# Performance work log

Measured on AMD Instinct MI355X. Metric: run time of the kernel, lower is better.

The kernel has to match this reference:

```python
import jax, jax.numpy as jnp
import numpy as np
jax.config.update("jax_enable_x64", True)

T_OLD = 60000
T_NEW = 60000
NV = 30000
MAX_STEPS = 300
FB_CHUNK = 500  # T_OLD must be divisible by this

FACE_OPP = np.array([[1, 2, 3], [0, 2, 3], [0, 1, 3], [0, 1, 2]])
EDGES = [(0, 1), (0, 2), (0, 3), (1, 2), (1, 3), (2, 3)]


def setup_inputs() -> dict:
    key = jax.random.key(0)
    k1, k2, k3, k4, k5 = jax.random.split(key, 5)
    # distinct vertices per tet (sorted base + strictly increasing offsets)
    off = jnp.arange(4, dtype=jnp.int64)
    new_indices = jnp.sort(jax.random.randint(k1, (T_NEW, 4), 0, NV - 4, dtype=jnp.int64), axis=1) + off
    old_indices = jnp.sort(jax.random.randint(k2, (T_OLD, 4), 0, NV - 4, dtype=jnp.int64), axis=1) + off
    return {
        "new_indices": new_indices,
        "old_indices": old_indices,
        "old_cc": jax.random.normal(k3, (T_OLD, 3), dtype=jnp.float32),
        "new_cc": jax.random.normal(k4, (T_NEW, 3), dtype=jnp.float32),
        "vertex_positions": jax.random.uniform(k5, (NV, 3), dtype=jnp.float32),
    }


def _min_edge_length(verts, indices):
    p = verts[indices]  # (T,4,3)
    el = jnp.stack([jnp.linalg.norm(p[:, a] - p[:, b], axis=-1) for a, b in EDGES])
    return el.min(axis=0)


def _forward(new_indices, old_indices, old_cc, new_cc, vertex_positions):
    T_new = new_indices.shape[0]
    T_old = old_indices.shape[0]
    Vn = vertex_positions.shape[0]

    # --- 1. unchanged-tet detection via sorted-vertex int64 keys ---
    key4 = lambda s: ((s[:, 0] * Vn + s[:, 1]) * Vn + s[:, 2]) * Vn + s[:, 3]
    ok = key4(jnp.sort(old_indices, axis=1))
    nk = key4(jnp.sort(new_indices, axis=1))
    order = jnp.argsort(ok)
    sk = ok[order]
    pos = jnp.searchsorted(sk, nk, side='right') - 1
    posc = jnp.clip(pos, 0, T_old - 1)
    matched = jnp.where((pos >= 0) & (sk[posc] == nk), order[posc], -1)
    is_matched = matched >= 0
    matched_safe = jnp.maximum(matched, 0)

    # --- 2. face adjacency of old mesh (sorted face keys, adjacent-equal pairing) ---
    fi = jnp.sort(old_indices[:, FACE_OPP], axis=2)          # (T_old,4,3)
    fk = (fi[..., 0] * Vn + fi[..., 1]) * Vn + fi[..., 2]    # (T_old,4)
    all_keys = fk.T.reshape(-1)                              # f-major like the numpy concat
    all_tets = jnp.tile(jnp.arange(T_old), 4)
    all_locals = jnp.repeat(jnp.arange(4), T_old)
    o2 = jnp.argsort(all_keys)
    sk2, st, sl = all_keys[o2], all_tets[o2], all_locals[o2]
    same = sk2[:-1] == sk2[1:]
    neighbors = jnp.full((T_old, 4), -1, dtype=jnp.int64)
    neighbors = neighbors.at[jnp.where(same, st[:-1], T_old), sl[:-1]].set(st[1:], mode='drop')
    neighbors = neighbors.at[jnp.where(same, st[1:], T_old), sl[1:]].set(st[:-1], mode='drop')

    # --- 3. per-old-tet inverse edge matrix; degenerate tets get no neighbors ---
    verts = jax.lax.stop_gradient(vertex_positions).astype(jnp.float32)
    p = verts[old_indices]                                   # (T_old,4,3)
    v0 = p[:, 0]
    Tm = jnp.stack([p[:, 1] - v0, p[:, 2] - v0, p[:, 3] - v0], axis=-1)
    degen = jnp.abs(jnp.linalg.det(Tm)) < 1e-10
    Tinv = jnp.linalg.inv(jnp.where(degen[:, None, None], jnp.eye(3, dtype=Tm.dtype), Tm))
    neighbors = jnp.where(degen[:, None], -1, neighbors)

    prio = jnp.full((Vn,), -1, dtype=jnp.int64)
    ar = jnp.arange(T_old)
    for vi in range(4):
        prio = prio.at[old_indices[:, vi]].max(vi * T_old + ar)
    v2t = jnp.where(prio >= 0, prio % T_old, 0)

    # --- 5. barycentric walk (masked, all float inputs stop-gradiented; int outputs) ---
    cent = jax.lax.stop_gradient(verts[new_indices].mean(axis=1))  # (T_new,3)
    seed = v2t[new_indices[:, 0]]
    n_walk = jnp.sum(~is_matched)
    thr = jnp.maximum(jnp.int64(100), n_walk // 1000)

    def cond(state):
        step, cur, rem, act = state
        return (step < MAX_STEPS) & (jnp.sum(act) >= thr)

    def body(state):
        step, cur, rem, act = state
        rel = cent - v0[cur]
        bary = jnp.einsum('nij,nj->ni', Tinv[cur], rel)
        all_b = jnp.concatenate([(1.0 - bary.sum(axis=1))[:, None], bary], axis=1)
        conv = act & (all_b.min(axis=1) >= -1e-4)
        rem = jnp.where(conv, cur, rem)
        act = act & ~conv
        nb = neighbors[cur, jnp.argmin(all_b, axis=1)]
        at_bd = act & (nb < 0)
        rem = jnp.where(at_bd, cur, rem)
        act = act & ~at_bd
        cur = jnp.where(act, nb, cur)
        return (step + 1, cur, rem, act)

    _, cur, rem, act = jax.lax.while_loop(cond, body, (jnp.int64(0), seed, seed, ~is_matched))
    rem = jnp.where(act, cur, rem)

    # --- 6. nearest-centroid fallback for unfinished walks (gated, chunked) ---
    old_cents = jax.lax.stop_gradient(verts[old_indices].mean(axis=1))

    def fallback(_):
        p2 = (cent ** 2).sum(-1)
        c2 = (old_cents ** 2).sum(-1)
        def scan_body(carry, i):
            bd, bi = carry
            c = jax.lax.dynamic_slice(old_cents, (i * FB_CHUNK, 0), (FB_CHUNK, 3))
            cn = jax.lax.dynamic_slice(c2, (i * FB_CHUNK,), (FB_CHUNK,))
            d = p2[:, None] - 2.0 * (cent @ c.T) + cn[None, :]
            md = d.min(axis=1)
            mi = d.argmin(axis=1).astype(jnp.int64) + i * FB_CHUNK
            imp = md < bd
            return (jnp.where(imp, md, bd), jnp.where(imp, mi, bi)), None
        init = (jnp.full((T_new,), jnp.inf, dtype=jnp.float32), jnp.zeros((T_new,), dtype=jnp.int64))
        (bd, bi), _ = jax.lax.scan(scan_body, init, jnp.arange(T_old // FB_CHUNK))
        return bi

    fb = jax.lax.cond(jnp.sum(act) > 0, fallback, lambda _: jnp.zeros((T_new,), dtype=jnp.int64), None)
    rem = jnp.clip(jnp.where(act, fb, rem), 0, T_old - 1)
    remap = jnp.where(is_matched, matched_safe, rem)

    # --- 7. candidates: containing tet + 4 face neighbors ---
    face_nb = neighbors[remap]
    face_nb = jnp.where(face_nb >= 0, face_nb, remap[:, None])
    cands = jnp.concatenate([remap[:, None], face_nb], axis=1)            # (T_new,5)
    cands = jnp.where(is_matched[:, None], matched_safe[:, None], cands)

    # --- 8. overlap / circumcenter-distance weights ---
    cand_verts = old_indices[cands]                                       # (T_new,5,4)
    overlap = (cand_verts[:, :, :, None] == new_indices[:, None, None, :]).any(-1).sum(-1).astype(jnp.float32)
    cc_d2 = ((old_cc[cands] - new_cc[:, None, :]) ** 2).sum(-1)
    raw = jnp.exp(overlap * 2.0) / (cc_d2 + 1e-8)
    weights = raw / raw.sum(axis=1, keepdims=True)

    # --- 9. density scale: min-edge-length ratio ---
    old_el = _min_edge_length(vertex_positions, old_indices)[cands]
    new_el = _min_edge_length(vertex_positions, new_indices)
    density_scale = jnp.clip(old_el / jnp.maximum(new_el[:, None], 1e-8), 0.1, 10.0)

    return cands, weights, density_scale


_forward_jit = jax.jit(_forward)


def reference(new_indices, old_indices, old_cc, new_cc, vertex_positions):
    return _forward_jit(new_indices, old_indices, old_cc, new_cc, vertex_positions)
```

## Files before the change

### kernel.cpp

```cpp
#include <hip/hip_runtime.h>

#pragma clang fp contract(off)

#define TOLD 60000
#define TNEW 60000
#define NVERT 30000
#define MAXSTEPS 300
#define THSZ 131072
#define FHSZ 131072
#define EMPTY64 0xFFFFFFFFFFFFFFFFULL

#define NB_SETUP 235
#define NB_NEWG  235
#define NB_FACE  938
#define NB_MATCH 235
#define NB_FB    120
#define FBRANGE  (TNEW / NB_FB)

#define OFF_TKEYS    0u
#define OFF_FTAB     1048576u
#define OFF_NBR      2097152u
#define OFF_PRIO     3057152u
#define FF_BYTES     3177152u
#define OFF_CNT      3177152u
#define OFF_TVALS    3179200u
#define OFF_IDXOLD   3703552u
#define OFF_SSTEP    4663552u
#define OFF_DEGEN    4903552u
#define OFF_MATCHED  5143552u
#define OFF_TV4      5383552u
#define OFF_COLD4    8263552u
#define OFF_CNEW4    9223552u
#define OFF_DM       10183552u

struct P {
  const unsigned int* rawNew;
  const unsigned int* rawOld;
  const float* occ;
  const float* ncc;
  const float* verts;
  float* out;
  unsigned long long* tkeys;
  unsigned long long* ftab;
  int* counters;
  int* tvals;
  int* idxOld;
  int* nbr;
  int* prio;
  int* sstep;
  int* degen;
  int* matched;
  float4* Tv4;
  float4* cold4;
  float4* cnew4;
  unsigned long long* dm;
  unsigned int dmMask;
};

__device__ __forceinline__ unsigned hash64(unsigned long long k){
  k ^= k >> 33; k *= 0xff51afd7ed558ccdULL;
  k ^= k >> 33; k *= 0xc4ceb9fe1a85ec53ULL;
  k ^= k >> 33;
  return (unsigned)k;
}
__device__ __forceinline__ void cswap(int& a, int& b){ if (a > b){ int t = a; a = b; b = t; } }

__device__ __forceinline__ int detect64(const unsigned int* raw){
  unsigned acc = 0;
  const uint4* r4 = (const uint4*)raw;
  #pragma unroll
  for (int k = 0; k < 32; ++k){ uint4 v = r4[k]; acc |= (v.y | v.w); }
  return acc == 0u;
}

__device__ __forceinline__ int4 load_tet4(const unsigned int* raw, int is64, int t){
  if (is64){
    uint4 a = ((const uint4*)raw)[t * 2 + 0];
    uint4 b = ((const uint4*)raw)[t * 2 + 1];
    return make_int4((int)a.x, (int)a.z, (int)b.x, (int)b.z);
  }
  uint4 a = ((const uint4*)raw)[t];
  return make_int4((int)a.x, (int)a.y, (int)a.z, (int)a.w);
}

__device__ __forceinline__ void face_insert(unsigned long long* ftab, int* nbr,
                                            unsigned long long fkey, int t, int l){
  unsigned long long mine = (fkey << 18) | (unsigned long long)(t * 4 + l);
  unsigned slot = hash64(fkey ^ 0x9e3779b97f4a7c15ULL) & (FHSZ - 1);
  while (true){
    unsigned long long prev = atomicCAS(&ftab[slot], EMPTY64, mine);
    if (prev == EMPTY64) return;
    if ((prev >> 18) == fkey){
      int oid = (int)(prev & 0x3FFFFULL);
      nbr[t * 4 + l] = oid >> 2;
      nbr[oid] = t;
      return;
    }
    slot = (slot + 1) & (FHSZ - 1);
  }
}

__device__ __forceinline__ float min_edge_r(
    float q0x, float q0y, float q0z, float q1x, float q1y, float q1z,
    float q2x, float q2y, float q2z, float q3x, float q3y, float q3z){
  float m = 3.402823466e+38f;
  float dx, dy, dz, d;
  dx = q0x - q1x; dy = q0y - q1y; dz = q0z - q1z; d = sqrtf((dx*dx + dy*dy) + dz*dz); m = fminf(m, d);
  dx = q0x - q2x; dy = q0y - q2y; dz = q0z - q2z; d = sqrtf((dx*dx + dy*dy) + dz*dz); m = fminf(m, d);
  dx = q0x - q3x; dy = q0y - q3y; dz = q0z - q3z; d = sqrtf((dx*dx + dy*dy) + dz*dz); m = fminf(m, d);
  dx = q1x - q2x; dy = q1y - q2y; dz = q1z - q2z; d = sqrtf((dx*dx + dy*dy) + dz*dz); m = fminf(m, d);
  dx = q1x - q3x; dy = q1y - q3y; dz = q1z - q3z; d = sqrtf((dx*dx + dy*dy) + dz*dz); m = fminf(m, d);
  dx = q2x - q3x; dy = q2y - q3y; dz = q2z - q3z; d = sqrtf((dx*dx + dy*dy) + dz*dz); m = fminf(m, d);
  return m;
}

__global__ __launch_bounds__(256) void k_front(P p){
  int bb = blockIdx.x;
  if (bb < NB_SETUP){
    int t = bb * 256 + threadIdx.x;
    if (bb == 0){
      for (int j = threadIdx.x; j < 384; j += 256) p.counters[j] = 0;
    }
    if (t >= TOLD) return;
    int is64 = detect64(p.rawOld);
    int4 iv4 = load_tet4(p.rawOld, is64, t);
    int i0 = iv4.x, i1 = iv4.y, i2 = iv4.z, i3 = iv4.w;
    ((int4*)p.idxOld)[t] = iv4;

    atomicMax(&p.prio[i0], 0 * TOLD + t);
    atomicMax(&p.prio[i1], 1 * TOLD + t);
    atomicMax(&p.prio[i2], 2 * TOLD + t);
    atomicMax(&p.prio[i3], 3 * TOLD + t);

    {
      int s0 = i0, s1 = i1, s2 = i2, s3 = i3;
      cswap(s0, s1); cswap(s2, s3); cswap(s0, s2); cswap(s1, s3); cswap(s1, s2);
      unsigned long long key =
          (unsigned long long)((((long long)s0 * NVERT + s1) * NVERT + s2) * NVERT + s3);
      unsigned slot = hash64(key) & (THSZ - 1);
      while (true){
        unsigned long long prev = atomicCAS(&p.tkeys[slot], EMPTY64, key);
        if (prev == EMPTY64){ p.tvals[slot] = t; break; }
        if (prev == key){ atomicMax(&p.tvals[slot], t); break; }
        slot = (slot + 1) & (THSZ - 1);
      }
    }

    if (p.dmMask){
      const int FO[4][3] = {{1, 2, 3}, {0, 2, 3}, {0, 1, 3}, {0, 1, 2}};
      int iv[4] = {i0, i1, i2, i3};
      #pragma unroll
      for (int l = 0; l < 4; ++l){
        int a = iv[FO[l][0]], b = iv[FO[l][1]], c = iv[FO[l][2]];
        cswap(a, b); cswap(a, c); cswap(b, c);
        unsigned long long fk = (unsigned long long)(((long long)a * NVERT + b) * NVERT + c);
        p.dm[hash64(fk) & p.dmMask] = (fk << 18) | (unsigned long long)(t * 4 + l);
      }
    }

    float q0x = p.verts[i0 * 3 + 0], q0y = p.verts[i0 * 3 + 1], q0z = p.verts[i0 * 3 + 2];
    float q1x = p.verts[i1 * 3 + 0], q1y = p.verts[i1 * 3 + 1], q1z = p.verts[i1 * 3 + 2];
    float q2x = p.verts[i2 * 3 + 0], q2y = p.verts[i2 * 3 + 1], q2z = p.verts[i2 * 3 + 2];
    float q3x = p.verts[i3 * 3 + 0], q3y = p.verts[i3 * 3 + 1], q3z = p.verts[i3 * 3 + 2];
    float e1x = q1x - q0x, e1y = q1y - q0y, e1z = q1z - q0z;
    float e2x = q2x - q0x, e2y = q2y - q0y, e2z = q2z - q0z;
    float e3x = q3x - q0x, e3y = q3y - q0y, e3z = q3z - q0z;
    float c23x = e2y * e3z - e2z * e3y;
    float c23y = e2z * e3x - e2x * e3z;
    float c23z = e2x * e3y - e2y * e3x;
    float det = e1x * c23x + e1y * c23y + e1z * c23z;
    int dg = (fabsf(det) < 1e-10f) ? 1 : 0;
    p.degen[t] = dg;
    float4 r0, r1, r2;
    if (dg){
      r0 = make_float4(1.f, 0.f, 0.f, q0x);
      r1 = make_float4(0.f, 1.f, 0.f, q0y);
      r2 = make_float4(0.f, 0.f, 1.f, q0z);
    } else {
      float inv = 1.0f / det;
      float c31x = e3y * e1z - e3z * e1y;
      float c31y = e3z * e1x - e3x * e1z;
      float c31z = e3x * e1y - e3y * e1x;
      float c12x = e1y * e2z - e1z * e2y;
      float c12y = e1z * e2x - e1x * e2z;
      float c12z = e1x * e2y - e1y * e2x;
      r0 = make_float4(c23x * inv, c23y * inv, c23z * inv, q0x);
      r1 = make_float4(c31x * inv, c31y * inv, c31z * inv, q0y);
      r2 = make_float4(c12x * inv, c12y * inv, c12z * inv, q0z);
    }
    p.Tv4[t * 3 + 0] = r0;
    p.Tv4[t * 3 + 1] = r1;
    p.Tv4[t * 3 + 2] = r2;
    float el = min_edge_r(q0x, q0y, q0z, q1x, q1y, q1z, q2x, q2y, q2z, q3x, q3y, q3z);
    p.cold4[t] = make_float4((((q0x + q1x) + q2x) + q3x) * 0.25f,
                             (((q0y + q1y) + q2y) + q3y) * 0.25f,
                             (((q0z + q1z) + q2z) + q3z) * 0.25f, el);
  } else {
    int n = (bb - NB_SETUP) * 256 + threadIdx.x;
    if (n >= TNEW) return;
    int is64 = detect64(p.rawNew);
    int4 ni = load_tet4(p.rawNew, is64, n);
    float q0x = p.verts[ni.x * 3 + 0], q0y = p.verts[ni.x * 3 + 1], q0z = p.verts[ni.x * 3 + 2];
    float q1x = p.verts[ni.y * 3 + 0], q1y = p.verts[ni.y * 3 + 1], q1z = p.verts[ni.y * 3 + 2];
    float q2x = p.verts[ni.z * 3 + 0], q2y = p.verts[ni.z * 3 + 1], q2z = p.verts[ni.z * 3 + 2];
    float q3x = p.verts[ni.w * 3 + 0], q3y = p.verts[ni.w * 3 + 1], q3z = p.verts[ni.w * 3 + 2];
    float el = min_edge_r(q0x, q0y, q0z, q1x, q1y, q1z, q2x, q2y, q2z, q3x, q3y, q3z);
    p.cnew4[n] = make_float4((((q0x + q1x) + q2x) + q3x) * 0.25f,
                             (((q0y + q1y) + q2y) + q3y) * 0.25f,
                             (((q0z + q1z) + q2z) + q3z) * 0.25f, el);
  }
}

__global__ __launch_bounds__(256) void k_mid(P p){
  int bb = blockIdx.x;
  if (bb < NB_FACE){
    int i = bb * 256 + threadIdx.x;
    if (i >= TOLD * 4) return;
    int t = i >> 2, l = i & 3;
    int4 iv4 = ((const int4*)p.idxOld)[t];
    int iv[4] = {iv4.x, iv4.y, iv4.z, iv4.w};
    const int FO[4][3] = {{1, 2, 3}, {0, 2, 3}, {0, 1, 3}, {0, 1, 2}};
    int a = iv[FO[l][0]], b = iv[FO[l][1]], c = iv[FO[l][2]];
    cswap(a, b); cswap(a, c); cswap(b, c);
    unsigned long long fk = (unsigned long long)(((long long)a * NVERT + b) * NVERT + c);
    if (p.dmMask){
      unsigned long long mine = (fk << 18) | (unsigned long long)i;
      unsigned long long got = p.dm[hash64(fk) & p.dmMask];
      if (got == mine) return;
      if ((got >> 18) == fk){
        int wid = (int)(got & 0x3FFFFULL);
        p.nbr[i] = wid >> 2;
        p.nbr[wid] = t;
        return;
      }
    }
    face_insert(p.ftab, p.nbr, fk, t, l);
  } else {
    int n = (bb - NB_FACE) * 256 + threadIdx.x;
    if (n >= TNEW) return;
    int is64 = detect64(p.rawNew);
    int4 ni = load_tet4(p.rawNew, is64, n);
    int s0 = ni.x, s1 = ni.y, s2 = ni.z, s3 = ni.w;
    cswap(s0, s1); cswap(s2, s3); cswap(s0, s2); cswap(s1, s3); cswap(s1, s2);
    unsigned long long key =
        (unsigned long long)((((long long)s0 * NVERT + s1) * NVERT + s2) * NVERT + s3);
    int m = -1;
    unsigned slot = hash64(key) & (THSZ - 1);
    while (true){
      unsigned long long k = p.tkeys[slot];
      if (k == EMPTY64) break;
      if (k == key){ m = p.tvals[slot]; break; }
      slot = (slot + 1) & (THSZ - 1);
    }
    p.matched[n] = m;
  }
}

__device__ __forceinline__ void assemble_walker(const P& p, int n, int m, int remap){
  int cds[5];
  if (m >= 0){
    cds[0] = cds[1] = cds[2] = cds[3] = cds[4] = m;
  } else {
    cds[0] = remap;
    int dg = p.degen[remap];
    int4 nb4 = ((const int4*)p.nbr)[remap];
    int nbl[4] = {nb4.x, nb4.y, nb4.z, nb4.w};
    for (int l = 0; l < 4; ++l){
      int fb = dg ? -1 : nbl[l];
      cds[1 + l] = (fb >= 0) ? fb : remap;
    }
  }
  bool same = (cds[1] == cds[0]) & (cds[2] == cds[0]) &
              (cds[3] == cds[0]) & (cds[4] == cds[0]);
  int is64 = detect64(p.rawNew);
  int4 ni = load_tet4(p.rawNew, is64, n);
  float nc0 = p.ncc[n * 3 + 0], nc1 = p.ncc[n * 3 + 1], nc2 = p.ncc[n * 3 + 2];
  float nelv = fmaxf(p.cnew4[n].w, 1e-8f);
  if (same){
    int ct = cds[0];
    int4 cv = ((const int4*)p.idxOld)[ct];
    int ov = 0;
    ov += (cv.x == ni.x || cv.x == ni.y || cv.x == ni.z || cv.x == ni.w) ? 1 : 0;
    ov += (cv.y == ni.x || cv.y == ni.y || cv.y == ni.z || cv.y == ni.w) ? 1 : 0;
    ov += (cv.z == ni.x || cv.z == ni.y || cv.z == ni.z || cv.z == ni.w) ? 1 : 0;
    ov += (cv.w == ni.x || cv.w == ni.y || cv.w == ni.z || cv.w == ni.w) ? 1 : 0;
    float d0 = p.occ[ct * 3 + 0] - nc0;
    float d1 = p.occ[ct * 3 + 1] - nc1;
    float d2 = p.occ[ct * 3 + 2] - nc2;
    float ccd2 = (d0 * d0 + d1 * d1) + d2 * d2;
    float raw = expf((float)ov * 2.0f) / (ccd2 + 1e-8f);
    float rsum = 0.0f;
    rsum += raw; rsum += raw; rsum += raw; rsum += raw; rsum += raw;
    float wgt = raw / rsum;
    float ds = p.cold4[ct].w / nelv;
    ds = fminf(fmaxf(ds, 0.1f), 10.0f);
    float cf = (float)ct;
    for (int c = 0; c < 5; ++c){
      p.out[n * 5 + c] = cf;
      p.out[TNEW * 5 + n * 5 + c] = wgt;
      p.out[2 * TNEW * 5 + n * 5 + c] = ds;
    }
    return;
  }
  float raws[5]; float rsum = 0.0f;
  float oels[5];
  for (int c = 0; c < 5; ++c){
    int ct = cds[c];
    int4 cv = ((const int4*)p.idxOld)[ct];
    int ov = 0;
    ov += (cv.x == ni.x || cv.x == ni.y || cv.x == ni.z || cv.x == ni.w) ? 1 : 0;
    ov += (cv.y == ni.x || cv.y == ni.y || cv.y == ni.z || cv.y == ni.w) ? 1 : 0;
    ov += (cv.z == ni.x || cv.z == ni.y || cv.z == ni.z || cv.z == ni.w) ? 1 : 0;
    ov += (cv.w == ni.x || cv.w == ni.y || cv.w == ni.z || cv.w == ni.w) ? 1 : 0;
    float d0 = p.occ[ct * 3 + 0] - nc0;
    float d1 = p.occ[ct * 3 + 1] - nc1;
    float d2 = p.occ[ct * 3 + 2] - nc2;
    float ccd2 = (d0 * d0 + d1 * d1) + d2 * d2;
    float raw = expf((float)ov * 2.0f) / (ccd2 + 1e-8f);
    raws[c] = raw; rsum += raw;
    oels[c] = p.cold4[ct].w;
  }
  for (int c = 0; c < 5; ++c){
    p.out[n * 5 + c] = (float)cds[c];
    p.out[TNEW * 5 + n * 5 + c] = raws[c] / rsum;
    float ds = oels[c] / nelv;
    ds = fminf(fmaxf(ds, 0.1f), 10.0f);
    p.out[2 * TNEW * 5 + n * 5 + c] = ds;
  }
}

__global__ __launch_bounds__(256) void k_walkall(P p){
  __shared__ int s_hist[MAXSTEPS + 2];
  __shared__ int s_nw;
  for (int j = threadIdx.x; j < MAXSTEPS + 2; j += 256) s_hist[j] = 0;
  if (threadIdx.x == 0) s_nw = 0;
  __syncthreads();
  int n = blockIdx.x * blockDim.x + threadIdx.x;
  if (n < TNEW){
    int m = p.matched[n];
    if (m >= 0){
      assemble_walker(p, n, m, 0);
    } else {
      atomicAdd(&s_nw, 1);
      int is64 = detect64(p.rawNew);
      int i0 = is64 ? (int)((const long long*)p.rawNew)[n * 4] : ((const int*)p.rawNew)[n * 4];
      int pr = p.prio[i0];
      int c = (pr >= 0) ? (pr % TOLD) : 0;
      float4 cn = p.cnew4[n];
      int s = MAXSTEPS + 1;
      for (int k = 1; k <= MAXSTEPS; ++k){
        float4 r0 = p.Tv4[c * 3 + 0];
        float4 r1 = p.Tv4[c * 3 + 1];
        float4 r2 = p.Tv4[c * 3 + 2];
        float rx = cn.x - r0.w, ry = cn.y - r1.w, rz = cn.z - r2.w;
        float b0 = r0.x * rx + r0.y * ry + r0.z * rz;
        float b1 = r1.x * rx + r1.y * ry + r1.z * rz;
        float b2 = r2.x * rx + r2.y * ry + r2.z * rz;
        float a0 = 1.0f - (b0 + b1 + b2);
        float ab[4] = {a0, b0, b1, b2};
        int amin = 0; float mn = ab[0];
        for (int j = 1; j < 4; ++j){ if (ab[j] < mn){ mn = ab[j]; amin = j; } }
        if (mn >= -0.0001f){ s = k; break; }
        int nb = p.degen[c] ? -1 : p.nbr[c * 4 + amin];
        if (nb < 0){ s = k; break; }
        c = nb;
      }
      p.sstep[n] = s;
      atomicAdd(&s_hist[s], 1);
      assemble_walker(p, n, -1, c);
    }
  }
  __syncthreads();
  if (threadIdx.x == 0 && s_nw) atomicAdd(&p.counters[0], s_nw);
  for (int j = threadIdx.x; j < MAXSTEPS + 2; j += 256){
    int v = s_hist[j];
    if (v) atomicAdd(&p.counters[64 + j], v);
  }
}

__device__ __forceinline__ int compute_S(const int* counters){
  int nw = counters[0];
  int thr = max(100, nw / 1000);
  if (nw < thr) return 0;
  int cnt = nw;
  for (int k = 1; k <= MAXSTEPS; ++k){
    cnt -= counters[64 + k];
    if (cnt < thr) return k;
  }
  return MAXSTEPS;
}

__global__ __launch_bounds__(256) void k_tail(P p){
  __shared__ float sd[256];
  __shared__ int si[256];
  __shared__ int s_hits[256];
  __shared__ int s_nhits;
  __shared__ int s_S;
  if (threadIdx.x == 0) s_S = compute_S(p.counters);
  __syncthreads();
  int S = s_S;
  int base = blockIdx.x * FBRANGE;
  for (int chunk = base; chunk < base + FBRANGE; chunk += 256){
    if (threadIdx.x == 0) s_nhits = 0;
    __syncthreads();
    int n = chunk + threadIdx.x;
    if (n < base + FBRANGE && n < TNEW){
      if (p.matched[n] < 0 && p.sstep[n] > S)
        s_hits[atomicAdd(&s_nhits, 1)] = n;
    }
    __syncthreads();
    int nh = s_nhits;
    for (int h = 0; h < nh; ++h){
      int n2 = s_hits[h];
      float4 cn = p.cnew4[n2];
      float cx = cn.x, cy = cn.y, cz = cn.z;
      float p2 = (cx * cx + cy * cy) + cz * cz;
      float bd = 3.402823466e+38f; int bi = 0;
      for (int j = threadIdx.x; j < TOLD; j += 256){
        float4 oc = p.cold4[j];
        float dot = (cx * oc.x + cy * oc.y) + cz * oc.z;
        float c2 = (oc.x * oc.x + oc.y * oc.y) + oc.z * oc.z;
        float d = (p2 - 2.0f * dot) + c2;
        if (d < bd || (d == bd && j < bi)){ bd = d; bi = j; }
      }
      sd[threadIdx.x] = bd; si[threadIdx.x] = bi;
      __syncthreads();
      for (int s = 128; s > 0; s >>= 1){
        if ((int)threadIdx.x < s){
          float od = sd[threadIdx.x + s]; int oi = si[threadIdx.x + s];
          if (od < sd[threadIdx.x] || (od == sd[threadIdx.x] && oi < si[threadIdx.x])){
            sd[threadIdx.x] = od; si[threadIdx.x] = oi;
          }
        }
        __syncthreads();
      }
      if (threadIdx.x == 0){
        int r = si[0];
        if (r < 0) r = 0; if (r > TOLD - 1) r = TOLD - 1;
        assemble_walker(p, n2, -1, r);
      }
      __syncthreads();
    }
    __syncthreads();
  }
}

extern "C" void kernel_launch(void* const* d_in, const int* in_sizes, int n_in,
                              void* d_out, int out_size, void* d_ws, size_t ws_size,
                              hipStream_t stream) {
  char* w = (char*)d_ws;
  P p;
  p.rawNew = (const unsigned int*)d_in[0];
  p.rawOld = (const unsigned int*)d_in[1];
  p.occ    = (const float*)d_in[2];
  p.ncc    = (const float*)d_in[3];
  p.verts  = (const float*)d_in[4];
  p.out    = (float*)d_out;
  p.tkeys    = (unsigned long long*)(w + OFF_TKEYS);
  p.ftab     = (unsigned long long*)(w + OFF_FTAB);
  p.nbr      = (int*)(w + OFF_NBR);
  p.prio     = (int*)(w + OFF_PRIO);
  p.counters = (int*)(w + OFF_CNT);
  p.tvals    = (int*)(w + OFF_TVALS);
  p.idxOld   = (int*)(w + OFF_IDXOLD);
  p.sstep    = (int*)(w + OFF_SSTEP);
  p.degen    = (int*)(w + OFF_DEGEN);
  p.matched  = (int*)(w + OFF_MATCHED);
  p.Tv4      = (float4*)(w + OFF_TV4);
  p.cold4    = (float4*)(w + OFF_COLD4);
  p.cnew4    = (float4*)(w + OFF_CNEW4);
  p.dm       = (unsigned long long*)(w + OFF_DM);
  size_t avail = (ws_size > (size_t)OFF_DM) ? ws_size - (size_t)OFF_DM : 0;
  unsigned dmMask = 0;
  for (int bshift = 21; bshift >= 16; --bshift){
    if (avail >= ((size_t)8 << bshift)){ dmMask = (1u << bshift) - 1u; break; }
  }
  p.dmMask = dmMask;

  hipMemsetAsync(w, 0xFF, FF_BYTES, stream);
  hipLaunchKernelGGL(k_front,   dim3(NB_SETUP + NB_NEWG), dim3(256), 0, stream, p);
  hipLaunchKernelGGL(k_mid,     dim3(NB_FACE + NB_MATCH), dim3(256), 0, stream, p);
  hipLaunchKernelGGL(k_walkall, dim3((TNEW + 255) / 256), dim3(256), 0, stream, p);
  hipLaunchKernelGGL(k_tail,    dim3(NB_FB), dim3(256), 0, stream, p);
}
```

Measured before the change: 116.5 us.

## Fold workspace memset into front kernel and move tet matching into walk kernel

```diff
diff --git a/kernel.cpp b/kernel.cpp
--- a/kernel.cpp
+++ b/kernel.cpp
@@ -12,8 +12,9 @@
 
 #define NB_SETUP 235
 #define NB_NEWG  235
+#define NB_INIT  194
 #define NB_FACE  938
-#define NB_MATCH 235
+#define NB_WALK  235
 #define NB_FB    120
 #define FBRANGE  (TNEW / NB_FB)
 
@@ -22,12 +23,12 @@
 #define OFF_NBR      2097152u
 #define OFF_PRIO     3057152u
 #define FF_BYTES     3177152u
+#define FF_UINT4     198572u
 #define OFF_CNT      3177152u
 #define OFF_TVALS    3179200u
 #define OFF_IDXOLD   3703552u
 #define OFF_SSTEP    4663552u
 #define OFF_DEGEN    4903552u
-#define OFF_MATCHED  5143552u
 #define OFF_TV4      5383552u
 #define OFF_COLD4    8263552u
 #define OFF_CNEW4    9223552u
@@ -49,7 +50,6 @@
   int* prio;
   int* sstep;
   int* degen;
-  int* matched;
   float4* Tv4;
   float4* cold4;
   float4* cnew4;
@@ -117,34 +117,15 @@
 __global__ __launch_bounds__(256) void k_front(P p){
   int bb = blockIdx.x;
   if (bb < NB_SETUP){
-    int t = bb * 256 + threadIdx.x;
     if (bb == 0){
       for (int j = threadIdx.x; j < 384; j += 256) p.counters[j] = 0;
     }
+    int t = bb * 256 + threadIdx.x;
     if (t >= TOLD) return;
     int is64 = detect64(p.rawOld);
     int4 iv4 = load_tet4(p.rawOld, is64, t);
     int i0 = iv4.x, i1 = iv4.y, i2 = iv4.z, i3 = iv4.w;
     ((int4*)p.idxOld)[t] = iv4;
-
-    atomicMax(&p.prio[i0], 0 * TOLD + t);
-    atomicMax(&p.prio[i1], 1 * TOLD + t);
-    atomicMax(&p.prio[i2], 2 * TOLD + t);
-    atomicMax(&p.prio[i3], 3 * TOLD + t);
-
-    {
-      int s0 = i0, s1 = i1, s2 = i2, s3 = i3;
-      cswap(s0, s1); cswap(s2, s3); cswap(s0, s2); cswap(s1, s3); cswap(s1, s2);
-      unsigned long long key =
-          (unsigned long long)((((long long)s0 * NVERT + s1) * NVERT + s2) * NVERT + s3);
-      unsigned slot = hash64(key) & (THSZ - 1);
-      while (true){
-        unsigned long long prev = atomicCAS(&p.tkeys[slot], EMPTY64, key);
-        if (prev == EMPTY64){ p.tvals[slot] = t; break; }
-        if (prev == key){ atomicMax(&p.tvals[slot], t); break; }
-        slot = (slot + 1) & (THSZ - 1);
-      }
-    }
 
     if (p.dmMask){
       const int FO[4][3] = {{1, 2, 3}, {0, 2, 3}, {0, 1, 3}, {0, 1, 2}};
@@ -195,7 +176,7 @@
     p.cold4[t] = make_float4((((q0x + q1x) + q2x) + q3x) * 0.25f,
                              (((q0y + q1y) + q2y) + q3y) * 0.25f,
                              (((q0z + q1z) + q2z) + q3z) * 0.25f, el);
-  } else {
+  } else if (bb < NB_SETUP + NB_NEWG){
     int n = (bb - NB_SETUP) * 256 + threadIdx.x;
     if (n >= TNEW) return;
     int is64 = detect64(p.rawNew);
@@ -208,55 +189,63 @@
     p.cnew4[n] = make_float4((((q0x + q1x) + q2x) + q3x) * 0.25f,
                              (((q0y + q1y) + q2y) + q3y) * 0.25f,
                              (((q0z + q1z) + q2z) + q3z) * 0.25f, el);
+  } else {
+    unsigned idx = (unsigned)(bb - NB_SETUP - NB_NEWG) * 1024u + threadIdx.x * 4u;
+    uint4 ff = make_uint4(~0u, ~0u, ~0u, ~0u);
+    uint4* base = (uint4*)p.tkeys;
+    #pragma unroll
+    for (unsigned k = 0; k < 4; ++k){
+      unsigned id = idx + k;
+      if (id < FF_UINT4) base[id] = ff;
+    }
   }
 }
 
 __global__ __launch_bounds__(256) void k_mid(P p){
-  int bb = blockIdx.x;
-  if (bb < NB_FACE){
-    int i = bb * 256 + threadIdx.x;
-    if (i >= TOLD * 4) return;
-    int t = i >> 2, l = i & 3;
-    int4 iv4 = ((const int4*)p.idxOld)[t];
-    int iv[4] = {iv4.x, iv4.y, iv4.z, iv4.w};
-    const int FO[4][3] = {{1, 2, 3}, {0, 2, 3}, {0, 1, 3}, {0, 1, 2}};
-    int a = iv[FO[l][0]], b = iv[FO[l][1]], c = iv[FO[l][2]];
-    cswap(a, b); cswap(a, c); cswap(b, c);
-    unsigned long long fk = (unsigned long long)(((long long)a * NVERT + b) * NVERT + c);
-    if (p.dmMask){
-      unsigned long long mine = (fk << 18) | (unsigned long long)i;
-      unsigned long long got = p.dm[hash64(fk) & p.dmMask];
-      if (got == mine) return;
-      if ((got >> 18) == fk){
-        int wid = (int)(got & 0x3FFFFULL);
-        p.nbr[i] = wid >> 2;
-        p.nbr[wid] = t;
-        return;
-      }
-    }
-    face_insert(p.ftab, p.nbr, fk, t, l);
-  } else {
-    int n = (bb - NB_FACE) * 256 + threadIdx.x;
-    if (n >= TNEW) return;
-    int is64 = detect64(p.rawNew);
-    int4 ni = load_tet4(p.rawNew, is64, n);
-    int s0 = ni.x, s1 = ni.y, s2 = ni.z, s3 = ni.w;
+  int i = blockIdx.x * 256 + threadIdx.x;
+  if (i >= TOLD * 4) return;
+  int t = i >> 2, l = i & 3;
+  int4 iv4 = ((const int4*)p.idxOld)[t];
+  int iv[4] = {iv4.x, iv4.y, iv4.z, iv4.w};
+
+  if (l == 0){
+    atomicMax(&p.prio[iv4.x], 0 * TOLD + t);
+    atomicMax(&p.prio[iv4.y], 1 * TOLD + t);
+    atomicMax(&p.prio[iv4.z], 2 * TOLD + t);
+    atomicMax(&p.prio[iv4.w], 3 * TOLD + t);
+    int s0 = iv4.x, s1 = iv4.y, s2 = iv4.z, s3 = iv4.w;
     cswap(s0, s1); cswap(s2, s3); cswap(s0, s2); cswap(s1, s3); cswap(s1, s2);
     unsigned long long key =
         (unsigned long long)((((long long)s0 * NVERT + s1) * NVERT + s2) * NVERT + s3);
-    int m = -1;
     unsigned slot = hash64(key) & (THSZ - 1);
     while (true){
-      unsigned long long k = p.tkeys[slot];
-      if (k == EMPTY64) break;
-      if (k == key){ m = p.tvals[slot]; break; }
+      unsigned long long prev = atomicCAS(&p.tkeys[slot], EMPTY64, key);
+      if (prev == EMPTY64){ p.tvals[slot] = t; break; }
+      if (prev == key){ atomicMax(&p.tvals[slot], t); break; }
       slot = (slot + 1) & (THSZ - 1);
     }
-    p.matched[n] = m;
-  }
-}
-
-__device__ __forceinline__ void assemble_walker(const P& p, int n, int m, int remap){
+  }
+
+  const int FO[4][3] = {{1, 2, 3}, {0, 2, 3}, {0, 1, 3}, {0, 1, 2}};
+  int a = iv[FO[l][0]], b = iv[FO[l][1]], c = iv[FO[l][2]];
+  cswap(a, b); cswap(a, c); cswap(b, c);
+  unsigned long long fk = (unsigned long long)(((long long)a * NVERT + b) * NVERT + c);
+  if (p.dmMask){
+    unsigned long long mine = (fk << 18) | (unsigned long long)i;
+    unsigned long long got = p.dm[hash64(fk) & p.dmMask];
+    if (got == mine) return;
+    if ((got >> 18) == fk){
+      int wid = (int)(got & 0x3FFFFULL);
+      p.nbr[i] = wid >> 2;
+      p.nbr[wid] = t;
+      return;
+    }
+  }
+  face_insert(p.ftab, p.nbr, fk, t, l);
+}
+
+__device__ __forceinline__ void assemble_walker(const P& p, int n, int m, int remap,
+                                                int4 ni){
   int cds[5];
   if (m >= 0){
     cds[0] = cds[1] = cds[2] = cds[3] = cds[4] = m;
@@ -272,8 +261,6 @@
   }
   bool same = (cds[1] == cds[0]) & (cds[2] == cds[0]) &
               (cds[3] == cds[0]) & (cds[4] == cds[0]);
-  int is64 = detect64(p.rawNew);
-  int4 ni = load_tet4(p.rawNew, is64, n);
   float nc0 = p.ncc[n * 3 + 0], nc1 = p.ncc[n * 3 + 1], nc2 = p.ncc[n * 3 + 2];
   float nelv = fmaxf(p.cnew4[n].w, 1e-8f);
   if (same){
@@ -337,14 +324,28 @@
   __syncthreads();
   int n = blockIdx.x * blockDim.x + threadIdx.x;
   if (n < TNEW){
-    int m = p.matched[n];
+    int is64 = detect64(p.rawNew);
+    int4 ni = load_tet4(p.rawNew, is64, n);
+    int m = -1;
+    {
+      int s0 = ni.x, s1 = ni.y, s2 = ni.z, s3 = ni.w;
+      cswap(s0, s1); cswap(s2, s3); cswap(s0, s2); cswap(s1, s3); cswap(s1, s2);
+      unsigned long long key =
+          (unsigned long long)((((long long)s0 * NVERT + s1) * NVERT + s2) * NVERT + s3);
+      unsigned slot = hash64(key) & (THSZ - 1);
+      while (true){
+        unsigned long long k = p.tkeys[slot];
+        if (k == EMPTY64) break;
+        if (k == key){ m = p.tvals[slot]; break; }
+        slot = (slot + 1) & (THSZ - 1);
+      }
+    }
     if (m >= 0){
-      assemble_walker(p, n, m, 0);
+      p.sstep[n] = 0;
+      assemble_walker(p, n, m, 0, ni);
     } else {
       atomicAdd(&s_nw, 1);
-      int is64 = detect64(p.rawNew);
-      int i0 = is64 ? (int)((const long long*)p.rawNew)[n * 4] : ((const int*)p.rawNew)[n * 4];
-      int pr = p.prio[i0];
+      int pr = p.prio[ni.x];
       int c = (pr >= 0) ? (pr % TOLD) : 0;
       float4 cn = p.cnew4[n];
       int s = MAXSTEPS + 1;
@@ -367,7 +368,7 @@
       }
       p.sstep[n] = s;
       atomicAdd(&s_hist[s], 1);
-      assemble_walker(p, n, -1, c);
+      assemble_walker(p, n, -1, c, ni);
     }
   }
   __syncthreads();
@@ -405,7 +406,7 @@
     __syncthreads();
     int n = chunk + threadIdx.x;
     if (n < base + FBRANGE && n < TNEW){
-      if (p.matched[n] < 0 && p.sstep[n] > S)
+      if (p.sstep[n] > S)
         s_hits[atomicAdd(&s_nhits, 1)] = n;
     }
     __syncthreads();
@@ -437,7 +438,9 @@
       if (threadIdx.x == 0){
         int r = si[0];
         if (r < 0) r = 0; if (r > TOLD - 1) r = TOLD - 1;
-        assemble_walker(p, n2, -1, r);
+        int is64 = detect64(p.rawNew);
+        int4 ni = load_tet4(p.rawNew, is64, n2);
+        assemble_walker(p, n2, -1, r, ni);
       }
       __syncthreads();
     }
@@ -465,7 +468,6 @@
   p.idxOld   = (int*)(w + OFF_IDXOLD);
   p.sstep    = (int*)(w + OFF_SSTEP);
   p.degen    = (int*)(w + OFF_DEGEN);
-  p.matched  = (int*)(w + OFF_MATCHED);
   p.Tv4      = (float4*)(w + OFF_TV4);
   p.cold4    = (float4*)(w + OFF_COLD4);
   p.cnew4    = (float4*)(w + OFF_CNEW4);
@@ -477,9 +479,8 @@
   }
   p.dmMask = dmMask;
 
-  hipMemsetAsync(w, 0xFF, FF_BYTES, stream);
-  hipLaunchKernelGGL(k_front,   dim3(NB_SETUP + NB_NEWG), dim3(256), 0, stream, p);
-  hipLaunchKernelGGL(k_mid,     dim3(NB_FACE + NB_MATCH), dim3(256), 0, stream, p);
-  hipLaunchKernelGGL(k_walkall, dim3((TNEW + 255) / 256), dim3(256), 0, stream, p);
+  hipLaunchKernelGGL(k_front,   dim3(NB_SETUP + NB_NEWG + NB_INIT), dim3(256), 0, stream, p);
+  hipLaunchKernelGGL(k_mid,     dim3(NB_FACE), dim3(256), 0, stream, p);
+  hipLaunchKernelGGL(k_walkall, dim3(NB_WALK), dim3(256), 0, stream, p);
   hipLaunchKernelGGL(k_tail,    dim3(NB_FB), dim3(256), 0, stream, p);
 }
```

Measured after the change: 115.8 us. About the same (-0.6%).
